# Kernel tuning notes

Measured on AMD Instinct MI355X. Metric: run time of the kernel, lower is better.

## Reference

```python
import jax, jax.numpy as jnp
import numpy as np

DIM = 1024
HEADS = 16
B, N = 4, 1024

def setup_inputs() -> dict:
    key = jax.random.key(0)
    k1, k2, k3 = jax.random.split(key, 3)
    x = jax.random.normal(k1, (B, N, DIM), dtype=jnp.float32)
    # xavier-uniform-ish init scale
    Wqkv = jax.random.normal(k2, (3 * DIM, DIM), dtype=jnp.float32) * (1.0 / np.sqrt(DIM))
    bqkv = jnp.zeros((3 * DIM,), dtype=jnp.float32)
    W1 = jax.random.normal(k3, (DIM, DIM), dtype=jnp.float32) * (1.0 / np.sqrt(DIM))
    b1 = jnp.zeros((DIM,), dtype=jnp.float32)
    return {"x": x, "Wqkv": Wqkv, "bqkv": bqkv, "W1": W1, "b1": b1}

def reference(x, Wqkv, bqkv, W1, b1):
    b, n, dim = x.shape
    h = HEADS
    d = dim // h
    scale = dim ** (-0.5)  # NOTE: module scales by full dim, not head dim
    qkv = x @ Wqkv.T + bqkv  # [b, n, 3*dim]
    qkv = qkv.reshape(b, n, 3, h, d)
    q = jnp.transpose(qkv[:, :, 0], (0, 2, 1, 3))  # [b, h, n, d]
    k = jnp.transpose(qkv[:, :, 1], (0, 2, 1, 3))
    v = jnp.transpose(qkv[:, :, 2], (0, 2, 1, 3))
    dots = jnp.einsum('bhid,bhjd->bhij', q, k) * scale
    attn = jax.nn.softmax(dots, axis=-1)
    out = jnp.einsum('bhij,bhjd->bhid', attn, v)
    out = jnp.transpose(out, (0, 2, 1, 3)).reshape(b, n, dim)
    out = out @ W1.T + b1
    return out
```

## Files before the change

### kernel.cpp

```cpp
#include <hip/hip_runtime.h>
#include <cmath>

typedef __bf16 bf16;
typedef __bf16 bf16x8 __attribute__((ext_vector_type(8)));
typedef __bf16 bf16x4 __attribute__((ext_vector_type(4)));
typedef float f32x4 __attribute__((ext_vector_type(4)));

#define MFMA16(a, b, c) __builtin_amdgcn_mfma_f32_16x16x32_bf16(a, b, c, 0, 0, 0)

__device__ __forceinline__ void load_lds16(const void* g, void* l) {
    __builtin_amdgcn_global_load_lds(
        (const __attribute__((address_space(1))) void*)g,
        (__attribute__((address_space(3))) void*)l, 16, 0, 0);
}

__device__ __forceinline__ bf16x8 load8(const bf16* p) { return *(const bf16x8*)p; }
__device__ __forceinline__ bf16x8 load8(const float* p) {
    float4 f0 = *(const float4*)p;
    float4 f1 = *(const float4*)(p + 4);
    bf16x8 r;
    r[0] = (bf16)f0.x; r[1] = (bf16)f0.y; r[2] = (bf16)f0.z; r[3] = (bf16)f0.w;
    r[4] = (bf16)f1.x; r[5] = (bf16)f1.y; r[6] = (bf16)f1.z; r[7] = (bf16)f1.w;
    return r;
}

__global__ __launch_bounds__(256) void cvt3(
    const float* __restrict__ s0, bf16* __restrict__ d0, int n0,
    const float* __restrict__ s1, bf16* __restrict__ d1, int n1,
    const float* __restrict__ s2, bf16* __restrict__ d2, int n2)
{
    int i = blockIdx.x * 256 + threadIdx.x;
    const float* s; bf16* d; int base;
    if (i < n0)                { s = s0; d = d0; base = i; }
    else if (i < n0 + n1)      { s = s1; d = d1; base = i - n0; }
    else if (i < n0 + n1 + n2) { s = s2; d = d2; base = i - n0 - n1; }
    else return;
    *(bf16x8*)(d + (size_t)base * 8) = load8(s + (size_t)base * 8);
}

template <int EPI, typename TB, int BN>
__global__ __launch_bounds__(256) void gemm_bt(
    const bf16* __restrict__ A, const TB* __restrict__ Bm,
    const float* __restrict__ bias,
    bf16* __restrict__ qo, bf16* __restrict__ ko, bf16* __restrict__ vto,
    float* __restrict__ C, int M, int N, int K)
{
    constexpr int WN = BN / 2;
    constexpr int JN = WN / 16;
    constexpr int SLOTS = (128 + BN) * 8;

    __shared__ bf16 As[128 * 64];
    __shared__ bf16 Bs[BN * 64];

    const int tid = threadIdx.x;
    const int l   = tid & 63;
    const int w   = tid >> 6;
    const int wm  = w & 1, wn = w >> 1;
    const int l15 = l & 15;
    const int g   = l >> 4;
    const int swz = l15 & 7;
    const int m0  = blockIdx.y * 128;
    const int n0  = blockIdx.x * BN;

    f32x4 acc[4][JN] = {};

    for (int k0 = 0; k0 < K; k0 += 64) {
        __syncthreads();
        #pragma unroll
        for (int it = 0; it < SLOTS / 256; ++it) {
            int s = it * 256 + w * 64 + l;
            if (s < 1024) {
                int row = s >> 3, pc = s & 7;
                int lc  = pc ^ (row & 7);
                load_lds16(A + (size_t)(m0 + row) * K + k0 + lc * 8, &As[s * 8]);
            } else {
                int t = s - 1024;
                int row = t >> 3, pc = t & 7;
                int lc  = pc ^ (row & 7);
                if constexpr (sizeof(TB) == 2) {
                    load_lds16(Bm + (size_t)(n0 + row) * K + k0 + lc * 8, &Bs[t * 8]);
                } else {
                    *(bf16x8*)&Bs[t * 8] = load8(Bm + (size_t)(n0 + row) * K + k0 + lc * 8);
                }
            }
        }
        __syncthreads();
        #pragma unroll
        for (int kk = 0; kk < 64; kk += 32) {
            bf16x8 aF[4], bF[JN];
            #pragma unroll
            for (int i = 0; i < 4; ++i)
                aF[i] = *(const bf16x8*)&As[(wm * 64 + i * 16 + l15) * 64
                                            + ((((kk >> 3) + g) ^ swz) * 8)];
            #pragma unroll
            for (int j = 0; j < JN; ++j)
                bF[j] = *(const bf16x8*)&Bs[(wn * WN + j * 16 + l15) * 64
                                            + ((((kk >> 3) + g) ^ swz) * 8)];
            #pragma unroll
            for (int i = 0; i < 4; ++i)
                #pragma unroll
                for (int j = 0; j < JN; ++j)
                    acc[i][j] = MFMA16(aF[i], bF[j], acc[i][j]);
        }
    }

    #pragma unroll
    for (int j = 0; j < JN; ++j) {
        int gcol = n0 + wn * WN + j * 16 + l15;
        float bv = bias[gcol];
        if (EPI == 0) {
            int which = gcol >> 10;
            int h  = (gcol >> 6) & 15;
            int dd = gcol & 63;
            #pragma unroll
            for (int i = 0; i < 4; ++i) {
                #pragma unroll
                for (int r = 0; r < 4; ++r) {
                    int grow = m0 + wm * 64 + i * 16 + g * 4 + r;
                    int b    = grow >> 10;
                    int npos = grow & 1023;
                    float v  = acc[i][j][r] + bv;
                    size_t bh = (size_t)(b * 16 + h);
                    if (which == 0)
                        qo[(bh * 1024 + npos) * 64 + dd] = (bf16)v;
                    else if (which == 1)
                        ko[(bh * 1024 + npos) * 64 + dd] = (bf16)v;
                    else
                        vto[(bh * 64 + dd) * 1024 + npos] = (bf16)v;
                }
            }
        } else {
            #pragma unroll
            for (int i = 0; i < 4; ++i)
                #pragma unroll
                for (int r = 0; r < 4; ++r) {
                    int grow = m0 + wm * 64 + i * 16 + g * 4 + r;
                    C[(size_t)grow * N + gcol] = acc[i][j][r] + bv;
                }
        }
    }
}

__global__ __launch_bounds__(256) void attn_fused(
    const bf16* __restrict__ qb, const bf16* __restrict__ kb,
    const bf16* __restrict__ vtb, bf16* __restrict__ attn)
{
    __shared__ bf16 Ks[64 * 64];
    __shared__ bf16 Vts[64 * 64];
    __shared__ bf16 Ps[4][16][72];

    const int tid = threadIdx.x;
    const int l   = tid & 63;
    const int w   = tid >> 6;
    const int l15 = l & 15;
    const int g   = l >> 4;
    const int swz = l15 & 7;
    const int bid = blockIdx.x;
    const int bh  = bid & 63;
    const int qc  = bid >> 6;
    const int m0  = qc * 64;

    const bf16* q_bh  = qb  + (size_t)bh * 65536;
    const bf16* k_bh  = kb  + (size_t)bh * 65536;
    const bf16* vt_bh = vtb + (size_t)bh * 65536;

    bf16x8 qf[2];
    #pragma unroll
    for (int kk = 0; kk < 2; ++kk)
        qf[kk] = *(const bf16x8*)(q_bh + (size_t)(m0 + w * 16 + l15) * 64
                                  + kk * 32 + g * 8);

    f32x4 o[4] = {};
    float lsum = 0.f;

    const float C_EXP = 0.04508422f;

    for (int j0 = 0; j0 < 1024; j0 += 64) {
        __syncthreads();
        #pragma unroll
        for (int it = 0; it < 2; ++it) {
            int s   = it * 256 + w * 64 + l;
            int row = s >> 3, pc = s & 7;
            int lc  = pc ^ (row & 7);
            load_lds16(k_bh + (size_t)(j0 + row) * 64 + lc * 8, &Ks[s * 8]);
            load_lds16(vt_bh + (size_t)row * 1024 + j0 + lc * 8, &Vts[s * 8]);
        }
        __syncthreads();

        f32x4 s4[4] = {};
        #pragma unroll
        for (int kk = 0; kk < 2; ++kk) {
            bf16x8 kf[4];
            #pragma unroll
            for (int js = 0; js < 4; ++js)
                kf[js] = *(const bf16x8*)&Ks[(js * 16 + l15) * 64
                                             + (((kk * 4 + g) ^ swz) * 8)];
            #pragma unroll
            for (int js = 0; js < 4; ++js)
                s4[js] = MFMA16(kf[js], qf[kk], s4[js]);
        }

        #pragma unroll
        for (int js = 0; js < 4; ++js) {
            bf16x4 pk;
            float ps = 0.f;
            #pragma unroll
            for (int r = 0; r < 4; ++r) {
                float p = exp2f(s4[js][r] * C_EXP);
                ps += p;
                pk[r] = (bf16)p;
            }
            lsum += ps;
            *(bf16x4*)&Ps[w][l15][js * 16 + g * 4] = pk;
        }
        __syncthreads();

        #pragma unroll
        for (int kk = 0; kk < 2; ++kk) {
            bf16x8 vf[4];
            #pragma unroll
            for (int ns = 0; ns < 4; ++ns)
                vf[ns] = *(const bf16x8*)&Vts[(ns * 16 + l15) * 64
                                              + (((kk * 4 + g) ^ swz) * 8)];
            bf16x8 pf = *(const bf16x8*)&Ps[w][l15][kk * 32 + g * 8];
            #pragma unroll
            for (int ns = 0; ns < 4; ++ns)
                o[ns] = MFMA16(pf, vf[ns], o[ns]);
        }
    }

    float t = lsum;
    t += __shfl_xor(t, 16);
    t += __shfl_xor(t, 32);

    #pragma unroll
    for (int r = 0; r < 4; ++r) {
        float inv = 1.0f / __shfl(t, g * 4 + r);
        int grow = m0 + w * 16 + g * 4 + r;
        size_t obase = ((size_t)(bh >> 4) * 1024 + grow) * 1024 + (bh & 15) * 64;
        #pragma unroll
        for (int ns = 0; ns < 4; ++ns)
            attn[obase + ns * 16 + l15] = (bf16)(o[ns][r] * inv);
    }
}

extern "C" void kernel_launch(void* const* d_in, const int* in_sizes, int n_in,
                              void* d_out, int out_size, void* d_ws, size_t ws_size,
                              hipStream_t stream)
{
    const float* x    = (const float*)d_in[0];
    const float* Wqkv = (const float*)d_in[1];
    const float* bqkv = (const float*)d_in[2];
    const float* W1   = (const float*)d_in[3];
    const float* b1   = (const float*)d_in[4];
    float* out = (float*)d_out;

    const size_t SEG = (size_t)4 * 16 * 1024 * 64;
    bf16* xbf  = (bf16*)d_ws;
    bf16* qb   = xbf + SEG;
    bf16* kb   = qb + SEG;
    bf16* vtb  = kb + SEG;
    bf16* attnb = xbf;
    bf16* wqkvbf = vtb + SEG;
    bf16* w1bf   = wqkvbf + 3145728;

    const bool cw = ws_size >= (size_t)(5 * SEG) * sizeof(bf16);

    const int nx = 524288;
    const int nw = cw ? 393216 : 0;
    const int n1 = cw ? 131072 : 0;
    const int tot = nx + nw + n1;
    cvt3<<<dim3((tot + 255) / 256), 256, 0, stream>>>(
        x, xbf, nx, Wqkv, wqkvbf, nw, W1, w1bf, n1);

    if (cw)
        gemm_bt<0, bf16, 128><<<dim3(24, 32), 256, 0, stream>>>(
            xbf, wqkvbf, bqkv, qb, kb, vtb, nullptr, 4096, 3072, 1024);
    else
        gemm_bt<0, float, 128><<<dim3(24, 32), 256, 0, stream>>>(
            xbf, Wqkv, bqkv, qb, kb, vtb, nullptr, 4096, 3072, 1024);

    attn_fused<<<dim3(1024), 256, 0, stream>>>(qb, kb, vtb, attnb);

    if (cw)
        gemm_bt<1, bf16, 64><<<dim3(16, 32), 256, 0, stream>>>(
            attnb, w1bf, b1, nullptr, nullptr, nullptr, out, 4096, 1024, 1024);
    else
        gemm_bt<1, float, 64><<<dim3(16, 32), 256, 0, stream>>>(
            attnb, W1, b1, nullptr, nullptr, nullptr, out, 4096, 1024, 1024);
}
```

Before: 172.5 us.

## Process 32 query rows per warp in attention to reuse K/V tiles

Each warp of the attention kernel now handles two 16-row query sub-tiles, so a block covers 128 query rows and the grid halves to 512 blocks. K and V fragments are read from shared memory once per tile into registers and reused for both sub-tiles, which halves K/V global-to-LDS traffic and LDS fragment reads per query row. The row sum is now accumulated from the bf16-rounded probabilities, matching what is fed to the PV product. The cost is higher register pressure from the doubled accumulators and preloaded fragments, plus fewer blocks, which may lower occupancy and parallelism.

```diff
diff --git a/kernel.cpp b/kernel.cpp
--- a/kernel.cpp
+++ b/kernel.cpp
@@ -147,7 +147,7 @@
 {
     __shared__ bf16 Ks[64 * 64];
     __shared__ bf16 Vts[64 * 64];
-    __shared__ bf16 Ps[4][16][72];
+    __shared__ bf16 Ps[4][32][72];
 
     const int tid = threadIdx.x;
     const int l   = tid & 63;
@@ -158,28 +158,30 @@
     const int bid = blockIdx.x;
     const int bh  = bid & 63;
     const int qc  = bid >> 6;
-    const int m0  = qc * 64;
+    const int m0  = qc * 128 + w * 32;
 
     const bf16* q_bh  = qb  + (size_t)bh * 65536;
     const bf16* k_bh  = kb  + (size_t)bh * 65536;
     const bf16* vt_bh = vtb + (size_t)bh * 65536;
 
-    bf16x8 qf[2];
+    bf16x8 qf[2][2];
     #pragma unroll
-    for (int kk = 0; kk < 2; ++kk)
-        qf[kk] = *(const bf16x8*)(q_bh + (size_t)(m0 + w * 16 + l15) * 64
-                                  + kk * 32 + g * 8);
-
-    f32x4 o[4] = {};
-    float lsum = 0.f;
-
+    for (int mi = 0; mi < 2; ++mi)
+        #pragma unroll
+        for (int kk = 0; kk < 2; ++kk)
+            qf[mi][kk] = *(const bf16x8*)(q_bh
+                + (size_t)(m0 + mi * 16 + l15) * 64 + kk * 32 + g * 8);
+
+    f32x4 o[2][4] = {};
+    float lsum[2] = {0.f, 0.f};
     const float C_EXP = 0.04508422f;
 
-    for (int j0 = 0; j0 < 1024; j0 += 64) {
+    for (int jt = 0; jt < 16; ++jt) {
+        const int j0 = jt * 64;
         __syncthreads();
         #pragma unroll
         for (int it = 0; it < 2; ++it) {
-            int s   = it * 256 + w * 64 + l;
+            int s   = it * 256 + tid;
             int row = s >> 3, pc = s & 7;
             int lc  = pc ^ (row & 7);
             load_lds16(k_bh + (size_t)(j0 + row) * 64 + lc * 8, &Ks[s * 8]);
@@ -187,60 +189,67 @@
         }
         __syncthreads();
 
-        f32x4 s4[4] = {};
+        bf16x8 kf[2][4], vf[2][4];
+        #pragma unroll
+        for (int kk = 0; kk < 2; ++kk)
+            #pragma unroll
+            for (int js = 0; js < 4; ++js) {
+                int off = (js * 16 + l15) * 64 + (((kk * 4 + g) ^ swz) * 8);
+                kf[kk][js] = *(const bf16x8*)&Ks[off];
+                vf[kk][js] = *(const bf16x8*)&Vts[off];
+            }
+
+        #pragma unroll
+        for (int mi = 0; mi < 2; ++mi) {
+            f32x4 s4[4] = {};
+            #pragma unroll
+            for (int kk = 0; kk < 2; ++kk)
+                #pragma unroll
+                for (int js = 0; js < 4; ++js)
+                    s4[js] = MFMA16(kf[kk][js], qf[mi][kk], s4[js]);
+            float ls = 0.f;
+            #pragma unroll
+            for (int js = 0; js < 4; ++js) {
+                bf16x4 pk;
+                #pragma unroll
+                for (int r = 0; r < 4; ++r) {
+                    pk[r] = (bf16)exp2f(s4[js][r] * C_EXP);
+                    ls += (float)pk[r];
+                }
+                *(bf16x4*)&Ps[w][mi * 16 + l15][js * 16 + g * 4] = pk;
+            }
+            lsum[mi] += ls;
+        }
+        __syncthreads();
+
         #pragma unroll
         for (int kk = 0; kk < 2; ++kk) {
-            bf16x8 kf[4];
-            #pragma unroll
-            for (int js = 0; js < 4; ++js)
-                kf[js] = *(const bf16x8*)&Ks[(js * 16 + l15) * 64
-                                             + (((kk * 4 + g) ^ swz) * 8)];
-            #pragma unroll
-            for (int js = 0; js < 4; ++js)
-                s4[js] = MFMA16(kf[js], qf[kk], s4[js]);
-        }
-
-        #pragma unroll
-        for (int js = 0; js < 4; ++js) {
-            bf16x4 pk;
-            float ps = 0.f;
-            #pragma unroll
-            for (int r = 0; r < 4; ++r) {
-                float p = exp2f(s4[js][r] * C_EXP);
-                ps += p;
-                pk[r] = (bf16)p;
-            }
-            lsum += ps;
-            *(bf16x4*)&Ps[w][l15][js * 16 + g * 4] = pk;
-        }
-        __syncthreads();
-
-        #pragma unroll
-        for (int kk = 0; kk < 2; ++kk) {
-            bf16x8 vf[4];
+            bf16x8 pf[2];
+            #pragma unroll
+            for (int mi = 0; mi < 2; ++mi)
+                pf[mi] = *(const bf16x8*)&Ps[w][mi * 16 + l15][kk * 32 + g * 8];
+            #pragma unroll
+            for (int mi = 0; mi < 2; ++mi)
+                #pragma unroll
+                for (int ns = 0; ns < 4; ++ns)
+                    o[mi][ns] = MFMA16(pf[mi], vf[kk][ns], o[mi][ns]);
+        }
+    }
+
+    #pragma unroll
+    for (int mi = 0; mi < 2; ++mi) {
+        float t = lsum[mi];
+        t += __shfl_xor(t, 16);
+        t += __shfl_xor(t, 32);
+        #pragma unroll
+        for (int r = 0; r < 4; ++r) {
+            float inv = 1.0f / __shfl(t, g * 4 + r);
+            int grow = m0 + mi * 16 + g * 4 + r;
+            size_t obase = ((size_t)(bh >> 4) * 1024 + grow) * 1024 + (bh & 15) * 64;
             #pragma unroll
             for (int ns = 0; ns < 4; ++ns)
-                vf[ns] = *(const bf16x8*)&Vts[(ns * 16 + l15) * 64
-                                              + (((kk * 4 + g) ^ swz) * 8)];
-            bf16x8 pf = *(const bf16x8*)&Ps[w][l15][kk * 32 + g * 8];
-            #pragma unroll
-            for (int ns = 0; ns < 4; ++ns)
-                o[ns] = MFMA16(pf, vf[ns], o[ns]);
-        }
-    }
-
-    float t = lsum;
-    t += __shfl_xor(t, 16);
-    t += __shfl_xor(t, 32);
-
-    #pragma unroll
-    for (int r = 0; r < 4; ++r) {
-        float inv = 1.0f / __shfl(t, g * 4 + r);
-        int grow = m0 + w * 16 + g * 4 + r;
-        size_t obase = ((size_t)(bh >> 4) * 1024 + grow) * 1024 + (bh & 15) * 64;
-        #pragma unroll
-        for (int ns = 0; ns < 4; ++ns)
-            attn[obase + ns * 16 + l15] = (bf16)(o[ns][r] * inv);
+                attn[obase + ns * 16 + l15] = (bf16)(o[mi][ns][r] * inv);
+        }
     }
 }
 
@@ -280,7 +289,7 @@
         gemm_bt<0, float, 128><<<dim3(24, 32), 256, 0, stream>>>(
             xbf, Wqkv, bqkv, qb, kb, vtb, nullptr, 4096, 3072, 1024);
 
-    attn_fused<<<dim3(1024), 256, 0, stream>>>(qb, kb, vtb, attnb);
+    attn_fused<<<dim3(512), 256, 0, stream>>>(qb, kb, vtb, attnb);
 
     if (cw)
         gemm_bt<1, bf16, 64><<<dim3(16, 32), 256, 0, stream>>>(
```

After: 174.3 us. About the same (+1.0%).
